# Optimization experiments

Measured on AMD Instinct MI355X. Metric: run time of the kernel, lower is better.

## Reference

```python
import jax, jax.numpy as jnp
import numpy as np

DATA_MAX = 30.0
LOG_FACTOR = float(np.log(DATA_MAX + 1.0))
THRESHOLDS = np.array([0.1, 1.0, 2.0, 5.0, 8.0], dtype=np.float32)
HIGHS = np.array([1.0, 2.0, 5.0, 8.0, np.inf], dtype=np.float32)
LEVEL_WEIGHTS = np.array([0.1, 0.1, 0.2, 0.25, 0.35], dtype=np.float32)
TIME_WEIGHTS = np.array([0.0075, 0.02, 0.03, 0.04, 0.05, 0.06, 0.07, 0.08, 0.09, 0.1,
                         0.09, 0.08, 0.07, 0.06, 0.05, 0.04, 0.03, 0.02, 0.0075, 0.005],
                        dtype=np.float32)


def setup_inputs() -> dict:
    key = jax.random.key(0)
    k1, k2, k3 = jax.random.split(key, 3)
    shape = (2, 20, 480, 480)
    pred_norm = jax.random.uniform(k1, shape, dtype=jnp.float32)
    target_norm = jax.random.uniform(k2, shape, dtype=jnp.float32)
    mask = jax.random.uniform(k3, shape, dtype=jnp.float32)
    return {"pred_norm": pred_norm, "target_norm": target_norm, "mask": mask}


def _metscore(pred_norm, target_norm, mask):
    # de-normalize to physical space (mm)
    pred = jnp.clip(jnp.expm1(pred_norm * LOG_FACTOR), 0.0, None)
    target = jnp.clip(jnp.expm1(target_norm * LOG_FACTOR), 0.0, None)
    B, T, H, W = pred.shape
    N = B * H * W
    # flatten each timestep across batch+space: [T, N]
    p = jnp.transpose(pred, (1, 0, 2, 3)).reshape(T, N)
    t = jnp.transpose(target, (1, 0, 2, 3)).reshape(T, N)
    m = (jnp.transpose(mask, (1, 0, 2, 3)).reshape(T, N) > 0.5)
    mf = m.astype(p.dtype)

    thr = jnp.asarray(THRESHOLDS)
    highs = jnp.asarray(HIGHS)
    lw = jnp.asarray(LEVEL_WEIGHTS)

    # ---- per-timestep masked correlation (excluding double-zero pixels) ----
    dz = (p < thr[0]) & (t < thr[0])
    mc = (m & ~dz).astype(p.dtype)                       # [T,N]
    cnt = mc.sum(-1)                                      # [T]
    safe_cnt = jnp.maximum(cnt, 1.0)
    p_mean = (p * mc).sum(-1) / safe_cnt
    t_mean = (t * mc).sum(-1) / safe_cnt
    dp = (p - p_mean[:, None]) * mc
    dt = (t - t_mean[:, None]) * mc
    num = (dp * dt).sum(-1)
    den = jnp.sqrt((dp * dp).sum(-1) * (dt * dt).sum(-1))
    r_time = jnp.where(cnt > 0, jnp.clip(num / (den + 1e-6), -1.0, 1.0), 0.0)  # [T]

    # ---- threshold-bin membership [T, L, N] ----
    p_in = ((p[:, None, :] >= thr[None, :, None]) & (p[:, None, :] < highs[None, :, None])).astype(p.dtype)
    t_in = ((t[:, None, :] >= thr[None, :, None]) & (t[:, None, :] < highs[None, :, None])).astype(p.dtype)

    hits = jnp.einsum('tln,tln,tn->tl', p_in, t_in, mf)   # [T,L]
    p_tot = jnp.einsum('tln,tn->tl', p_in, mf)            # hits + false alarms
    t_tot = jnp.einsum('tln,tn->tl', t_in, mf)            # hits + misses
    ts_mat = hits / (p_tot + t_tot - hits + 1e-8)         # [T,L]

    diff = jnp.abs(p - t) * mf                            # [T,N]
    mae_num = jnp.einsum('tln,tn->tl', t_in, diff)
    mae_mat = jnp.where(t_tot > 0, mae_num / jnp.maximum(t_tot, 1.0), 0.0)  # [T,L]

    # ---- score combination ----
    term_corr = jnp.sqrt(jnp.exp(r_time - 1.0))           # [T]
    term_mae = jnp.sqrt(jnp.exp(-mae_mat / 100.0))        # [T,L]
    score_time = term_corr * (lw[None, :] * ts_mat * term_mae).sum(-1)  # [T]

    tw = jnp.asarray(TIME_WEIGHTS)
    if T == tw.shape[0]:
        w_time = tw
    elif T < tw.shape[0]:
        w_time = tw[:T] / tw[:T].sum()
    else:
        w_time = jnp.ones((T,), dtype=p.dtype) / T
    total = (score_time * w_time).sum()
    return total, score_time, r_time, ts_mat, mae_mat, ts_mat.mean(0), mae_mat.mean(0)


def reference(pred_norm, target_norm, mask):
    return _metscore(pred_norm, target_norm, mask)
```

## Files before the change

### kernel.cpp

```cpp
#include <hip/hip_runtime.h>
#include <math.h>

#define TS   20
#define NL   5
#define NS   26
#define GX   45
#define TPB  256
#define F4PT 5
#define HW4  57600

constexpr float C1 = (float)(0.09531017980432486 / 3.4339872044851463);
constexpr float C2 = (float)(0.69314718055994531 / 3.4339872044851463);
constexpr float C3 = (float)(1.09861228866810969 / 3.4339872044851463);
constexpr float C4 = (float)(1.79175946922805500 / 3.4339872044851463);
constexpr float C5 = (float)(2.19722457733621938 / 3.4339872044851463);

__device__ __forceinline__ float expm1_ln31(float x)
{
#if __has_builtin(__builtin_amdgcn_exp2f)
    return __builtin_amdgcn_exp2f(x * 4.9541963103868751f) - 1.0f;
#else
    return __expf(x * 3.4339872044851463f) - 1.0f;
#endif
}

__device__ __forceinline__ void px(float pn, float tn, float mn,
    unsigned& pP, unsigned& tP, unsigned& hP, int& cnt, float cum[NL],
    float& sp, float& st, float& spt, float& spp, float& stt)
{
    bool mok = mn > 0.5f;
    float pm = mok ? pn : -1.0f;
    float qm = mok ? tn : -1.0f;
    bool p1 = pm >= C1, p2 = pm >= C2, p3 = pm >= C3, p4 = pm >= C4, p5 = pm >= C5;
    bool q1 = qm >= C1, q2 = qm >= C2, q3 = qm >= C3, q4 = qm >= C4, q5 = qm >= C5;
    int lp = (int)p1 + (int)p2 + (int)p3 + (int)p4 + (int)p5;
    int lq = (int)q1 + (int)q2 + (int)q3 + (int)q4 + (int)q5;
    unsigned ohp = 1u << (5 * lp);
    pP += ohp;
    tP += 1u << (5 * lq);
    hP += (lp == lq) ? ohp : 0u;
    float p = expm1_ln31(pn);
    float q = expm1_ln31(tn);
    bool cond = (lp | lq) != 0;
    cnt += cond ? 1 : 0;
    float pz = cond ? p : 0.0f;
    float qz = cond ? q : 0.0f;
    sp += pz;  st += qz;
    spt = fmaf(pz, qz, spt);
    spp = fmaf(pz, pz, spp);
    stt = fmaf(qz, qz, stt);
    float ad = fabsf(p - q);
    cum[0] += q1 ? ad : 0.0f;
    cum[1] += q2 ? ad : 0.0f;
    cum[2] += q3 ? ad : 0.0f;
    cum[3] += q4 ? ad : 0.0f;
    cum[4] += q5 ? ad : 0.0f;
}

__global__ __launch_bounds__(TPB) void metscore_pass1(
    const float4* __restrict__ pred, const float4* __restrict__ targ,
    const float4* __restrict__ mask, float* __restrict__ sums )
{
    const int t = blockIdx.y;
    const int b = blockIdx.z;
    const size_t base = ((size_t)b * TS + t) * (size_t)HW4
                      + (size_t)blockIdx.x * (F4PT * TPB) + threadIdx.x;

    float4 P[F4PT], T[F4PT], M[F4PT];
    #pragma unroll
    for (int j = 0; j < F4PT; ++j) P[j] = pred[base + j * TPB];
    #pragma unroll
    for (int j = 0; j < F4PT; ++j) T[j] = targ[base + j * TPB];
    #pragma unroll
    for (int j = 0; j < F4PT; ++j) M[j] = mask[base + j * TPB];

    unsigned pP = 0u, tP = 0u, hP = 0u;
    int cnt = 0;
    float cum[NL] = {0, 0, 0, 0, 0};
    float sp = 0, st = 0, spt = 0, spp = 0, stt = 0;

    #pragma unroll
    for (int j = 0; j < F4PT; ++j) {
        px(P[j].x, T[j].x, M[j].x, pP, tP, hP, cnt, cum, sp, st, spt, spp, stt);
        px(P[j].y, T[j].y, M[j].y, pP, tP, hP, cnt, cum, sp, st, spt, spp, stt);
        px(P[j].z, T[j].z, M[j].z, pP, tP, hP, cnt, cum, sp, st, spt, spp, stt);
        px(P[j].w, T[j].w, M[j].w, pP, tP, hP, cnt, cum, sp, st, spt, spp, stt);
    }

    unsigned c16[8];
    #pragma unroll
    for (int k = 0; k < 8; ++k) c16[k] = 0u;
    #pragma unroll
    for (int l = 0; l < NL; ++l) {
        c16[l >> 1]        += ((hP >> (5 * (l + 1))) & 31u) << (16 * (l & 1));
        c16[(5 + l) >> 1]  += ((pP >> (5 * (l + 1))) & 31u) << (16 * ((5 + l) & 1));
        c16[(10 + l) >> 1] += ((tP >> (5 * (l + 1))) & 31u) << (16 * ((10 + l) & 1));
    }
    c16[7] += (unsigned)cnt << 16;

    float f[10] = {cum[0], cum[1], cum[2], cum[3], cum[4], sp, st, spt, spp, stt};
    #pragma unroll
    for (int k = 0; k < 8; ++k) {
        unsigned x = c16[k];
        x += __shfl_down(x, 32); x += __shfl_down(x, 16); x += __shfl_down(x, 8);
        x += __shfl_down(x, 4);  x += __shfl_down(x, 2);  x += __shfl_down(x, 1);
        c16[k] = x;
    }
    #pragma unroll
    for (int k = 0; k < 10; ++k) {
        float x = f[k];
        x += __shfl_down(x, 32); x += __shfl_down(x, 16); x += __shfl_down(x, 8);
        x += __shfl_down(x, 4);  x += __shfl_down(x, 2);  x += __shfl_down(x, 1);
        f[k] = x;
    }

    __shared__ unsigned ldsU[4][8];
    __shared__ float    ldsF[4][10];
    const int lane = threadIdx.x & 63;
    const int wv   = threadIdx.x >> 6;
    if (lane == 0) {
        #pragma unroll
        for (int k = 0; k < 8; ++k) ldsU[wv][k] = c16[k];
        #pragma unroll
        for (int k = 0; k < 10; ++k) ldsF[wv][k] = f[k];
    }
    __syncthreads();
    if (threadIdx.x < 8) {
        unsigned s = ldsU[0][threadIdx.x] + ldsU[1][threadIdx.x]
                   + ldsU[2][threadIdx.x] + ldsU[3][threadIdx.x];
        int c0 = 2 * threadIdx.x, c1 = c0 + 1;
        int n0 = (c0 == 15) ? 20 : c0;
        int n1 = (c1 == 15) ? 20 : c1;
        atomicAdd(&sums[t * NS + n0], (float)(s & 0xFFFFu));
        atomicAdd(&sums[t * NS + n1], (float)(s >> 16));
    } else if (threadIdx.x < 18) {
        int k = threadIdx.x - 8;
        float s = ldsF[0][k] + ldsF[1][k] + ldsF[2][k] + ldsF[3][k];
        int n = (k < 5) ? (15 + k) : (16 + k);
        atomicAdd(&sums[t * NS + n], s);
    }
}

__global__ __launch_bounds__(128) void metscore_final(
    const float* __restrict__ sums, float* __restrict__ out)
{
    __shared__ float ts_s[TS][NL];
    __shared__ float mae_s[TS][NL];
    __shared__ float sc_s[TS];
    const int tid = threadIdx.x;

    if (tid < TS * NL) {
        int tt_ = tid / NL, l = tid % NL;
        const float* s = sums + tt_ * NS;
        float h = s[l], pt = s[5 + l], tt = s[10 + l];
        float mn = s[15 + l] - ((l < NL - 1) ? s[16 + l] : 0.0f);
        float ts  = h / (pt + tt - h + 1e-8f);
        float mae = (tt > 0.0f) ? (mn / fmaxf(tt, 1.0f)) : 0.0f;
        ts_s[tt_][l]  = ts;
        mae_s[tt_][l] = mae;
        out[41 + tid]  = ts;
        out[141 + tid] = mae;
    }
    __syncthreads();

    if (tid < TS) {
        const float* s = sums + tid * NS;
        double cnt = s[20], sp = s[21], st = s[22];
        double spt = s[23], spp = s[24], stt = s[25];
        double sc = fmax(cnt, 1.0);
        double pmn = sp / sc, tmn = st / sc;
        double num = spt - pmn * st - tmn * sp + pmn * tmn * cnt;
        double vp  = spp - 2.0 * pmn * sp + pmn * pmn * cnt;
        double vt  = stt - 2.0 * tmn * st + tmn * tmn * cnt;
        double r = num / (sqrt(vp * vt) + 1e-6);
        r = fmin(fmax(r, -1.0), 1.0);
        float rt = (cnt > 0.0) ? (float)r : 0.0f;
        out[21 + tid] = rt;

        const float LW[NL] = {0.1f, 0.1f, 0.2f, 0.25f, 0.35f};
        float term_corr = sqrtf(expf(rt - 1.0f));
        float accl = 0.0f;
        #pragma unroll
        for (int l = 0; l < NL; ++l)
            accl += LW[l] * ts_s[tid][l] * sqrtf(expf(-mae_s[tid][l] * 0.01f));
        float sct = term_corr * accl;
        out[1 + tid] = sct;

        const float TW[TS] = {0.0075f, 0.02f, 0.03f, 0.04f, 0.05f, 0.06f, 0.07f,
                              0.08f, 0.09f, 0.1f, 0.09f, 0.08f, 0.07f, 0.06f,
                              0.05f, 0.04f, 0.03f, 0.02f, 0.0075f, 0.005f};
        sc_s[tid] = sct * TW[tid];
    }
    __syncthreads();

    if (tid == 0) {
        float tot = 0.0f;
        for (int k = 0; k < TS; ++k) tot += sc_s[k];
        out[0] = tot;
    }
    if (tid < NL) {
        float a = 0.0f, bsum = 0.0f;
        for (int k = 0; k < TS; ++k) { a += ts_s[k][tid]; bsum += mae_s[k][tid]; }
        out[241 + tid] = a * (1.0f / TS);
        out[246 + tid] = bsum * (1.0f / TS);
    }
}

extern "C" void kernel_launch(void* const* d_in, const int* in_sizes, int n_in,
                              void* d_out, int out_size, void* d_ws, size_t ws_size,
                              hipStream_t stream) {
    (void)in_sizes; (void)n_in; (void)out_size; (void)ws_size;
    const float4* pred = (const float4*)d_in[0];
    const float4* targ = (const float4*)d_in[1];
    const float4* mask = (const float4*)d_in[2];
    float* out  = (float*)d_out;
    float* sums = (float*)d_ws;

    hipMemsetAsync(sums, 0, TS * NS * sizeof(float), stream);

    dim3 grid(GX, TS, 2);
    metscore_pass1<<<grid, TPB, 0, stream>>>(pred, targ, mask, sums);
    metscore_final<<<1, 128, 0, stream>>>(sums, out);
}
```

Baseline: 143.0 us.

## Replace global atomics and memset with per-block partials reduced in final kernel

Each block now writes its reduced float and packed-count partials to a per-block slot in workspace instead of issuing float atomicAdds into a shared sums array. The final kernel gathers the partials across blocks and batches. This removes the memset launch and atomic contention. The grid is also enlarged (more blocks, fewer float4 per thread) for better occupancy. The cost is a longer serial gather loop in the single-block final kernel.

```diff
diff --git a/kernel.cpp b/kernel.cpp
--- a/kernel.cpp
+++ b/kernel.cpp
@@ -4,10 +4,11 @@
 #define TS   20
 #define NL   5
 #define NS   26
-#define GX   45
+#define GX   75
 #define TPB  256
-#define F4PT 5
+#define F4PT 3
 #define HW4  57600
+#define NPK  18
 
 constexpr float C1 = (float)(0.09531017980432486 / 3.4339872044851463);
 constexpr float C2 = (float)(0.69314718055994531 / 3.4339872044851463);
@@ -59,7 +60,8 @@
 
 __global__ __launch_bounds__(TPB) void metscore_pass1(
     const float4* __restrict__ pred, const float4* __restrict__ targ,
-    const float4* __restrict__ mask, float* __restrict__ sums )
+    const float4* __restrict__ mask, float* __restrict__ fpart,
+    unsigned* __restrict__ upart)
 {
     const int t = blockIdx.y;
     const int b = blockIdx.z;
@@ -125,33 +127,62 @@
         for (int k = 0; k < 10; ++k) ldsF[wv][k] = f[k];
     }
     __syncthreads();
-    if (threadIdx.x < 8) {
-        unsigned s = ldsU[0][threadIdx.x] + ldsU[1][threadIdx.x]
-                   + ldsU[2][threadIdx.x] + ldsU[3][threadIdx.x];
-        int c0 = 2 * threadIdx.x, c1 = c0 + 1;
-        int n0 = (c0 == 15) ? 20 : c0;
-        int n1 = (c1 == 15) ? 20 : c1;
-        atomicAdd(&sums[t * NS + n0], (float)(s & 0xFFFFu));
-        atomicAdd(&sums[t * NS + n1], (float)(s >> 16));
-    } else if (threadIdx.x < 18) {
-        int k = threadIdx.x - 8;
-        float s = ldsF[0][k] + ldsF[1][k] + ldsF[2][k] + ldsF[3][k];
-        int n = (k < 5) ? (15 + k) : (16 + k);
-        atomicAdd(&sums[t * NS + n], s);
-    }
-}
-
-__global__ __launch_bounds__(128) void metscore_final(
-    const float* __restrict__ sums, float* __restrict__ out)
-{
+
+    const size_t blk = ((size_t)b * TS + t) * GX + blockIdx.x;
+    if (threadIdx.x < 10) {
+        int k = threadIdx.x;
+        fpart[blk * NPK + k] = ldsF[0][k] + ldsF[1][k] + ldsF[2][k] + ldsF[3][k];
+    } else if (threadIdx.x < NPK) {
+        int k = threadIdx.x - 10;
+        upart[blk * NPK + threadIdx.x] = ldsU[0][k] + ldsU[1][k] + ldsU[2][k] + ldsU[3][k];
+    }
+}
+
+__global__ __launch_bounds__(768) void metscore_final(
+    const float* __restrict__ fpart, const unsigned* __restrict__ upart,
+    float* __restrict__ out)
+{
+    __shared__ float S[TS][NS];
     __shared__ float ts_s[TS][NL];
     __shared__ float mae_s[TS][NL];
     __shared__ float sc_s[TS];
     const int tid = threadIdx.x;
 
+    if (tid < 720) {
+        const int g = tid >> 1;
+        const int t = g / NPK;
+        const int k = g % NPK;
+        const int b = tid & 1;
+        const size_t base = (((size_t)b * TS + t) * GX) * NPK + k;
+        if (k < 10) {
+            float s = 0.0f;
+            for (int gx = 0; gx < GX; ++gx) s += fpart[base + (size_t)gx * NPK];
+            s += __shfl_down(s, 1);
+            if (b == 0) {
+                int n = (k < 5) ? (15 + k) : (16 + k);
+                S[t][n] = s;
+            }
+        } else {
+            unsigned lo = 0u, hi = 0u;
+            for (int gx = 0; gx < GX; ++gx) {
+                unsigned v = upart[base + (size_t)gx * NPK];
+                lo += v & 0xFFFFu;  hi += v >> 16;
+            }
+            lo += __shfl_down(lo, 1);
+            hi += __shfl_down(hi, 1);
+            if (b == 0) {
+                int j = k - 10;
+                int c0 = 2 * j, c1 = 2 * j + 1;
+                S[t][c0 == 15 ? 20 : c0] = (float)lo;
+                S[t][c1 == 15 ? 20 : c1] = (float)hi;
+            }
+        }
+    }
+    __syncthreads();
+
     if (tid < TS * NL) {
         int tt_ = tid / NL, l = tid % NL;
-        const float* s = sums + tt_ * NS;
+        const float* s = S[tt_];
         float h = s[l], pt = s[5 + l], tt = s[10 + l];
         float mn = s[15 + l] - ((l < NL - 1) ? s[16 + l] : 0.0f);
         float ts  = h / (pt + tt - h + 1e-8f);
@@ -164,7 +195,7 @@
     __syncthreads();
 
     if (tid < TS) {
-        const float* s = sums + tid * NS;
+        const float* s = S[tid];
         double cnt = s[20], sp = s[21], st = s[22];
         double spt = s[23], spp = s[24], stt = s[25];
         double sc = fmax(cnt, 1.0);
@@ -213,12 +244,11 @@
     const float4* pred = (const float4*)d_in[0];
     const float4* targ = (const float4*)d_in[1];
     const float4* mask = (const float4*)d_in[2];
-    float* out  = (float*)d_out;
-    float* sums = (float*)d_ws;
-
-    hipMemsetAsync(sums, 0, TS * NS * sizeof(float), stream);
+    float*    out   = (float*)d_out;
+    float*    fpart = (float*)d_ws;
+    unsigned* upart = (unsigned*)d_ws;
 
     dim3 grid(GX, TS, 2);
-    metscore_pass1<<<grid, TPB, 0, stream>>>(pred, targ, mask, sums);
-    metscore_final<<<1, 128, 0, stream>>>(sums, out);
-}
+    metscore_pass1<<<grid, TPB, 0, stream>>>(pred, targ, mask, fpart, upart);
+    metscore_final<<<1, 768, 0, stream>>>(fpart, upart, out);
+}
```

After: 146.1 us. 2.2% more time.
